# Performance work log

Measured on AMD Instinct MI355X. Metric: run time of the kernel, lower is better.

## Reference

```python
import jax, jax.numpy as jnp
import numpy as np

SFREQ = 100

def _std1(x, axis):
    # torch.std default: unbiased (ddof=1)
    return jnp.std(x, axis=axis, ddof=1)

def setup_inputs() -> dict:
    key = jax.random.key(0)
    eeg_data = jax.random.normal(key, (2048, 128, 500), dtype=jnp.float32)
    return {"eeg_data": eeg_data}

def reference(eeg_data):
    B, C, T = eeg_data.shape
    # --- P300 window: [T//3, 2T//3) ---
    p0, p1 = T // 3, 2 * T // 3
    p300 = eeg_data[:, :, p0:p1]                      # (B,C,Wp)
    peak_idx = jnp.argmax(p300, axis=-1)              # (B,C)
    lat = (p0 + peak_idx).astype(eeg_data.dtype) / SFREQ  # (B,C)
    amp = jnp.max(p300, axis=-1)                      # (B,C)
    p300_feats = jnp.stack([
        lat.mean(axis=1), _std1(lat, 1),
        amp.mean(axis=1), amp.max(axis=1),
        (amp * lat).mean(axis=1),
    ], axis=1)                                        # (B,5)
    # --- N200 window: [0.2T, 0.35T) ---
    n0, n1 = int(0.2 * T), int(0.35 * T)
    n2_amp = jnp.min(eeg_data[:, :, n0:n1], axis=-1)  # (B,C)
    n2_feats = jnp.stack([
        n2_amp.mean(axis=1), _std1(n2_amp, 1), n2_amp.min(axis=1),
    ], axis=1)                                        # (B,3)
    # --- alpha (prestim) power: [0, T//3) ---
    alpha_p = jnp.mean(eeg_data[:, :, :p0] ** 2, axis=-1)  # (B,C)
    alpha_feats = jnp.stack([
        alpha_p.mean(axis=1), _std1(alpha_p, 1), alpha_p.max(axis=1),
    ], axis=1)                                        # (B,3)
    # --- beta (motor) power: [T//3, 2T//3) ---
    beta_p = jnp.mean(p300 ** 2, axis=-1)             # (B,C)
    beta_feats = jnp.stack([
        beta_p.mean(axis=1), _std1(beta_p, 1),
    ], axis=1)                                        # (B,2)
    return jnp.concatenate([p300_feats, n2_feats, alpha_feats, beta_feats], axis=1)  # (B,13)
```

## Files before the change

### kernel.cpp

```cpp
#include <hip/hip_runtime.h>
#include <float.h>

#define NCH  128
#define TLEN 500
#define P0 166
#define P1 333
#define N0 100
#define N1 175

__device__ __forceinline__ float wave_sum(float v) {
#pragma unroll
    for (int m = 32; m; m >>= 1) v += __shfl_xor(v, m, 64);
    return v;
}
__device__ __forceinline__ float wave_min(float v) {
#pragma unroll
    for (int m = 32; m; m >>= 1) v = fminf(v, __shfl_xor(v, m, 64));
    return v;
}
__device__ __forceinline__ float wave_max(float v) {
#pragma unroll
    for (int m = 32; m; m >>= 1) v = fmaxf(v, __shfl_xor(v, m, 64));
    return v;
}

__global__ __launch_bounds__(256) void erp_feats_kernel(
    const float* __restrict__ eeg, float* __restrict__ out) {
    const int b    = blockIdx.x;
    const int tid  = threadIdx.x;
    const int wid  = tid >> 6;
    const int lane = tid & 63;
    const int g    = lane >> 4;
    const int l    = lane & 15;

    __shared__ float s_lat[NCH], s_amp[NCH], s_n2[NCH], s_alpha[NCH], s_beta[NCH];

    const float* __restrict__ base = eeg + (size_t)b * NCH * TLEN;

#pragma unroll
    for (int p = 0; p < 8; ++p) {
        const int c = p * 16 + wid * 4 + g;
        const float* __restrict__ ch = base + (size_t)c * TLEN;

        float asum  = 0.0f;
        float bsum  = 0.0f;
        float n2min = FLT_MAX;
        float pmax  = -FLT_MAX;
        int   pidx  = P0;

#pragma unroll
        for (int k = 0; k < 5; ++k) {
            const int i = k * 16 + l;
            const float4 v = *reinterpret_cast<const float4*>(ch + 4 * i);
            const float e[4] = {v.x, v.y, v.z, v.w};
            const int t0 = 4 * i;
#pragma unroll
            for (int j = 0; j < 4; ++j) {
                const int t = t0 + j;
                const float x  = e[j];
                const float xx = x * x;
                if (t < P0) {
                    asum += xx;
                } else {
                    bsum += xx;
                    if (x > pmax) { pmax = x; pidx = t; }
                }
                if (t >= N0 && t < N1) n2min = fminf(n2min, x);
            }
        }
        if (l < 4) {
            const int i = 80 + l;
            const float4 v = *reinterpret_cast<const float4*>(ch + 4 * i);
            const float e[4] = {v.x, v.y, v.z, v.w};
            const int t0 = 4 * i;
#pragma unroll
            for (int j = 0; j < 4; ++j) {
                const int t = t0 + j;
                if (t < P1) {
                    const float x = e[j];
                    bsum += x * x;
                    if (x > pmax) { pmax = x; pidx = t; }
                }
            }
        }

#pragma unroll
        for (int m = 8; m; m >>= 1) {
            asum  += __shfl_xor(asum, m, 64);
            bsum  += __shfl_xor(bsum, m, 64);
            n2min  = fminf(n2min, __shfl_xor(n2min, m, 64));
            const float om = __shfl_xor(pmax, m, 64);
            const int   oi = __shfl_xor(pidx, m, 64);
            if (om > pmax || (om == pmax && oi < pidx)) { pmax = om; pidx = oi; }
        }

        if (l == 0) {
            s_lat[c]   = (float)pidx / 100.0f;
            s_amp[c]   = pmax;
            s_n2[c]    = n2min;
            s_alpha[c] = asum / 166.0f;
            s_beta[c]  = bsum / 167.0f;
        }
    }

    __syncthreads();

    if (wid == 0) {
        const float lat0 = s_lat[lane],   lat1 = s_lat[lane + 64];
        const float amp0 = s_amp[lane],   amp1 = s_amp[lane + 64];
        const float n20  = s_n2[lane],    n21  = s_n2[lane + 64];
        const float al0  = s_alpha[lane], al1  = s_alpha[lane + 64];
        const float be0  = s_beta[lane],  be1  = s_beta[lane + 64];

        const float inv_n = 1.0f / 128.0f;
        const float inv_m = 1.0f / 127.0f;

        const float lat_mean = wave_sum(lat0 + lat1) * inv_n;
        const float amp_mean = wave_sum(amp0 + amp1) * inv_n;
        const float n2_mean  = wave_sum(n20 + n21)   * inv_n;
        const float al_mean  = wave_sum(al0 + al1)   * inv_n;
        const float be_mean  = wave_sum(be0 + be1)   * inv_n;
        const float axl_mean = wave_sum(amp0 * lat0 + amp1 * lat1) * inv_n;

        const float dl0 = lat0 - lat_mean, dl1 = lat1 - lat_mean;
        const float lat_std = sqrtf(wave_sum(dl0 * dl0 + dl1 * dl1) * inv_m);
        const float dn0 = n20 - n2_mean, dn1 = n21 - n2_mean;
        const float n2_std = sqrtf(wave_sum(dn0 * dn0 + dn1 * dn1) * inv_m);
        const float da0 = al0 - al_mean, da1 = al1 - al_mean;
        const float al_std = sqrtf(wave_sum(da0 * da0 + da1 * da1) * inv_m);
        const float db0 = be0 - be_mean, db1 = be1 - be_mean;
        const float be_std = sqrtf(wave_sum(db0 * db0 + db1 * db1) * inv_m);

        const float amp_max = wave_max(fmaxf(amp0, amp1));
        const float n2_min  = wave_min(fminf(n20, n21));
        const float al_max  = wave_max(fmaxf(al0, al1));

        if (lane == 0) {
            float* o = out + (size_t)b * 13;
            o[0]  = lat_mean;
            o[1]  = lat_std;
            o[2]  = amp_mean;
            o[3]  = amp_max;
            o[4]  = axl_mean;
            o[5]  = n2_mean;
            o[6]  = n2_std;
            o[7]  = n2_min;
            o[8]  = al_mean;
            o[9]  = al_std;
            o[10] = al_max;
            o[11] = be_mean;
            o[12] = be_std;
        }
    }
}

extern "C" void kernel_launch(void* const* d_in, const int* in_sizes, int n_in,
                              void* d_out, int out_size, void* d_ws, size_t ws_size,
                              hipStream_t stream) {
    const float* eeg = (const float*)d_in[0];
    float* out = (float*)d_out;
    const int B = in_sizes[0] / (NCH * TLEN);
    erp_feats_kernel<<<dim3(B), dim3(256), 0, stream>>>(eeg, out);
}
```

Before: 71.95 us.

## Use DPP row-rotate for 16-lane channel reductions and stop unrolling channel loop

Measured after the change: 72.39 us. No clear change (+0.6%).

```diff
diff --git a/kernel.cpp b/kernel.cpp
--- a/kernel.cpp
+++ b/kernel.cpp
@@ -7,6 +7,17 @@
 #define P1 333
 #define N0 100
 #define N1 175
+
+template<int CTRL>
+__device__ __forceinline__ float dpp_rorf(float v) {
+    const int s = __float_as_int(v);
+    const int d = __builtin_amdgcn_update_dpp(s, s, CTRL, 0xF, 0xF, false);
+    return __int_as_float(d);
+}
+template<int CTRL>
+__device__ __forceinline__ int dpp_rori(int v) {
+    return __builtin_amdgcn_update_dpp(v, v, CTRL, 0xF, 0xF, false);
+}
 
 __device__ __forceinline__ float wave_sum(float v) {
 #pragma unroll
@@ -37,7 +48,7 @@
 
     const float* __restrict__ base = eeg + (size_t)b * NCH * TLEN;
 
-#pragma unroll
+#pragma unroll 1
     for (int p = 0; p < 8; ++p) {
         const int c = p * 16 + wid * 4 + g;
         const float* __restrict__ ch = base + (size_t)c * TLEN;
@@ -84,15 +95,20 @@
             }
         }
 
-#pragma unroll
-        for (int m = 8; m; m >>= 1) {
-            asum  += __shfl_xor(asum, m, 64);
-            bsum  += __shfl_xor(bsum, m, 64);
-            n2min  = fminf(n2min, __shfl_xor(n2min, m, 64));
-            const float om = __shfl_xor(pmax, m, 64);
-            const int   oi = __shfl_xor(pidx, m, 64);
-            if (om > pmax || (om == pmax && oi < pidx)) { pmax = om; pidx = oi; }
+#define RED_STEP(CTRL)                                                       \
+        {                                                                    \
+            asum  += dpp_rorf<CTRL>(asum);                                   \
+            bsum  += dpp_rorf<CTRL>(bsum);                                   \
+            n2min  = fminf(n2min, dpp_rorf<CTRL>(n2min));                    \
+            const float om = dpp_rorf<CTRL>(pmax);                           \
+            const int   oi = dpp_rori<CTRL>(pidx);                           \
+            if (om > pmax || (om == pmax && oi < pidx)) { pmax = om; pidx = oi; } \
         }
+        RED_STEP(0x128)
+        RED_STEP(0x124)
+        RED_STEP(0x122)
+        RED_STEP(0x121)
+#undef RED_STEP
 
         if (l == 0) {
             s_lat[c]   = (float)pidx / 100.0f;
```
